# Optimization experiments

Measured on AMD Instinct MI355X. Metric: run time of the kernel, lower is better.

Reference implementation:

```python
import jax, jax.numpy as jnp
import numpy as np

N_NODES = 20000
N_EDGES = 640000
IN_DIM = 128
HID = 128
NUM_GRAPHS = 64


def setup_inputs() -> dict:
    key = jax.random.key(0)
    ks = jax.random.split(key, 12)
    x = jax.random.normal(ks[0], (N_NODES, IN_DIM), dtype=jnp.float32)
    edge_index = jax.random.randint(ks[1], (2, N_EDGES), 0, N_NODES, dtype=jnp.int64)
    batch = jnp.sort(jax.random.randint(ks[2], (N_NODES,), 0, NUM_GRAPHS, dtype=jnp.int64))
    edge_attr = jax.random.uniform(ks[3], (N_EDGES,), dtype=jnp.float32)
    s1 = 1.0 / np.sqrt(IN_DIM)
    s2 = 1.0 / np.sqrt(HID)
    # GraphConv layer 1: lin_rel (with bias) on aggregated messages, lin_root (no bias) on x
    W1_rel = jax.random.uniform(ks[4], (HID, IN_DIM), minval=-s1, maxval=s1, dtype=jnp.float32)
    b1 = jax.random.uniform(ks[5], (HID,), minval=-s1, maxval=s1, dtype=jnp.float32)
    W1_root = jax.random.uniform(ks[6], (HID, IN_DIM), minval=-s1, maxval=s1, dtype=jnp.float32)
    # GraphConv layer 3 (conv2 is unused in forward)
    W3_rel = jax.random.uniform(ks[7], (HID, HID), minval=-s2, maxval=s2, dtype=jnp.float32)
    b3 = jax.random.uniform(ks[8], (HID,), minval=-s2, maxval=s2, dtype=jnp.float32)
    W3_root = jax.random.uniform(ks[9], (HID, HID), minval=-s2, maxval=s2, dtype=jnp.float32)
    # Final linear head
    Wlin = jax.random.uniform(ks[10], (1, HID), minval=-s2, maxval=s2, dtype=jnp.float32)
    blin = jax.random.uniform(ks[11], (1,), minval=-s2, maxval=s2, dtype=jnp.float32)
    return {
        "x": x, "edge_index": edge_index, "batch": batch, "edge_attr": edge_attr,
        "W1_rel": W1_rel, "b1": b1, "W1_root": W1_root,
        "W3_rel": W3_rel, "b3": b3, "W3_root": W3_root,
        "Wlin": Wlin, "blin": blin, "num_graphs": NUM_GRAPHS,
    }


def graph_conv(x, src, dst, edge_w, W_rel, b_rel, W_root):
    # PyG GraphConv (aggr='add'): out = W_rel @ sum_{j in N(i)} w_ij * x_j + b_rel + W_root @ x_i
    msg = x[src] * edge_w[:, None]                       # [E, d] gather + scale
    agg = jax.ops.segment_sum(msg, dst, num_segments=x.shape[0])  # [N, d] scatter-add
    return agg @ W_rel.T + b_rel + x @ W_root.T


def reference(x, edge_index, batch, edge_attr,
              W1_rel, b1, W1_root, W3_rel, b3, W3_root, Wlin, blin, num_graphs):
    src, dst = edge_index[0], edge_index[1]
    h = graph_conv(x, src, dst, edge_attr, W1_rel, b1, W1_root)
    h = jax.nn.relu(h)
    # dropout p=0.5 is identity in eval mode
    h = graph_conv(h, src, dst, edge_attr, W3_rel, b3, W3_root)
    # global_mean_pool over per-node graph ids
    sums = jax.ops.segment_sum(h, batch, num_segments=num_graphs)          # [G, H]
    counts = jax.ops.segment_sum(jnp.ones((h.shape[0],), h.dtype), batch,
                                 num_segments=num_graphs)                  # [G]
    pooled = sums / jnp.maximum(counts, 1.0)[:, None]
    out = jax.nn.relu(pooled @ Wlin.T + blin)                              # [G, 1]
    return out
```

## Files before the change

### kernel.cpp

```cpp
#include <hip/hip_runtime.h>

#define N_NODES 20000
#define N_EDGES 640000
#define DIM 128
#define NGRAPH 64
#define NBUCK 313
#define EPB 2048
#define NB_HIST 313
#define NB_WCONV 32
#define RED_BLOCKS 512

typedef __attribute__((ext_vector_type(8))) short short8;
typedef __attribute__((ext_vector_type(4))) float floatx4;

__device__ __forceinline__ unsigned int bf16rne(float f) {
    unsigned int u = __float_as_uint(f);
    return (u + 0x7FFFu + ((u >> 16) & 1u)) >> 16;
}

__global__ __launch_bounds__(256) void k_front(
    const int* __restrict__ dst,
    const float* __restrict__ Wrel, const float* __restrict__ Wroot,
    const float* __restrict__ W3rel, const float* __restrict__ W3root,
    const float* __restrict__ b3, const float* __restrict__ Wlin,
    unsigned short* __restrict__ wbh, unsigned short* __restrict__ wbl,
    int* __restrict__ ghist, int* __restrict__ ticket_hist,
    int* __restrict__ boff, int* __restrict__ gcursor,
    float* __restrict__ vrel, float* __restrict__ vroot, float* __restrict__ cb3) {

    const int t = threadIdx.x;
    const int blk = blockIdx.x;

    if (blk < NB_HIST) {
        __shared__ int lhist[NBUCK];
        __shared__ int islast;
        for (int i = t; i < NBUCK; i += 256) lhist[i] = 0;
        __syncthreads();
        const int e0 = blk * EPB;
        for (int i = 0; i < 8; ++i) {
            int e = e0 + i * 256 + t;
            if (e < N_EDGES) atomicAdd(&lhist[dst[e] >> 6], 1);
        }
        __syncthreads();
        for (int i = t; i < NBUCK; i += 256)
            if (lhist[i]) atomicAdd(&ghist[i], lhist[i]);
        __syncthreads();
        if (t == 0) {
            __threadfence();
            islast = (atomicAdd(ticket_hist, 1) == NB_HIST - 1);
        }
        __syncthreads();
        if (islast) {
            __threadfence();
            if (t < 64) {
                int carry = 0;
                for (int c = 0; c < 5; ++c) {
                    int idx = c * 64 + t;
                    int v = (idx < NBUCK)
                        ? __hip_atomic_load(&ghist[idx], __ATOMIC_RELAXED,
                                            __HIP_MEMORY_SCOPE_AGENT)
                        : 0;
                    int xv = v;
                    for (int s = 1; s < 64; s <<= 1) {
                        int u = __shfl_up(xv, s);
                        if (t >= s) xv += u;
                    }
                    int excl = carry + xv - v;
                    if (idx < NBUCK) { boff[idx] = excl; gcursor[idx] = excl; }
                    carry += __shfl(xv, 63);
                }
                if (t == 0) boff[NBUCK] = carry;
            }
        }
    } else if (blk < NB_HIST + NB_WCONV) {
        const int b = blk - NB_HIST;
        for (int i = b * 256 + t; i < 256 * DIM; i += NB_WCONV * 256) {
            int n = i >> 7, k = i & 127;
            float v = (n < DIM) ? Wrel[n * DIM + k] : Wroot[(n - DIM) * DIM + k];
            unsigned int h = bf16rne(v);
            wbh[i] = (unsigned short)h;
            wbl[i] = (unsigned short)bf16rne(v - __uint_as_float(h << 16));
        }
    } else {
        if (t < 64) {
            for (int kk = 0; kk < 2; ++kk) {
                int k = t + kk * 64;
                float sr = 0.f, so = 0.f;
                for (int h = 0; h < DIM; ++h) {
                    float wl = Wlin[h];
                    sr = fmaf(wl, W3rel[h * DIM + k], sr);
                    so = fmaf(wl, W3root[h * DIM + k], so);
                }
                vrel[k] = sr;
                vroot[k] = so;
            }
            float c = b3[t] * Wlin[t] + b3[t + 64] * Wlin[t + 64];
            for (int m = 32; m > 0; m >>= 1) c += __shfl_xor(c, m);
            if (t == 0) cb3[0] = c;
        }
    }
}

__global__ __launch_bounds__(256) void k_partition(const int* __restrict__ src,
                                                   const int* __restrict__ dst,
                                                   const float* __restrict__ ew,
                                                   int* __restrict__ gcursor,
                                                   int2* __restrict__ part) {
    __shared__ int lhist[NBUCK], lbase[NBUCK], gbase[NBUCK], lcur[NBUCK];
    __shared__ int2 lrec[EPB];
    const int t = threadIdx.x;
    for (int i = t; i < NBUCK; i += 256) lhist[i] = 0;
    __syncthreads();
    const int e0 = blockIdx.x * EPB;
    const int tot = min(EPB, N_EDGES - e0);
    int mys[8], myd[8];
    float myw[8];
    for (int i = 0; i < 8; ++i) {
        int e = e0 + i * 256 + t;
        if (e < N_EDGES) {
            mys[i] = src[e];
            myd[i] = dst[e];
            myw[i] = ew[e];
            atomicAdd(&lhist[myd[i] >> 6], 1);
        } else {
            myd[i] = -1;
        }
    }
    __syncthreads();
    if (t < 64) {
        int carry = 0;
        for (int c = 0; c < 5; ++c) {
            int idx = c * 64 + t;
            int v = (idx < NBUCK) ? lhist[idx] : 0;
            int xv = v;
            for (int s = 1; s < 64; s <<= 1) {
                int u = __shfl_up(xv, s);
                if (t >= s) xv += u;
            }
            if (idx < NBUCK) { lbase[idx] = carry + xv - v; lcur[idx] = 0; }
            carry += __shfl(xv, 63);
        }
    }
    __syncthreads();
    for (int i = t; i < NBUCK; i += 256) {
        int cnt = lhist[i];
        gbase[i] = cnt ? atomicAdd(&gcursor[i], cnt) : 0;
    }
    __syncthreads();
    for (int i = 0; i < 8; ++i) {
        if (myd[i] >= 0) {
            int bb = myd[i] >> 6;
            int slot = lbase[bb] + atomicAdd(&lcur[bb], 1);
            lrec[slot] = make_int2((myd[i] << 16) | mys[i], __float_as_int(myw[i]));
        }
    }
    __syncthreads();
    for (int i = t; i < tot; i += 256) {
        int2 rc = lrec[i];
        int bb = (rc.x >> 16) >> 6;
        part[gbase[bb] + (i - lbase[bb])] = rc;
    }
}

__global__ __launch_bounds__(256) void k_gemm(
    const float* __restrict__ x,
    const unsigned short* __restrict__ wbh, const unsigned short* __restrict__ wbl,
    const float* __restrict__ b1,
    unsigned short* __restrict__ yb, float* __restrict__ r) {
    extern __shared__ unsigned short smem[];
    uint4* sh = (uint4*)smem;
    uint4* sl = (uint4*)(smem + 16384);

    const int t = threadIdx.x;
    const int g = blockIdx.x;
    const int half = blockIdx.y;
    const int n0 = half * 128;

    const uint4* gh = (const uint4*)wbh + (size_t)n0 * 16;
    const uint4* gl = (const uint4*)wbl + (size_t)n0 * 16;
    for (int i = t; i < 2048; i += 256) {
        int row = i >> 4, c = i & 15;
        int sc = row * 16 + (c ^ (row & 15));
        sh[sc] = gh[i];
        sl[sc] = gl[i];
    }
    __syncthreads();

    const int lane = t & 63;
    const int m = lane & 15;
    const int q = lane >> 4;
    const int row0 = g * 64 + (t >> 6) * 16;
    const int row = row0 + m;
    const bool ok = row < N_NODES;

    const short8* SH = (const short8*)smem;
    const short8* SL = (const short8*)(smem + 16384);

    floatx4 acc[8];
    #pragma unroll
    for (int i = 0; i < 8; ++i) acc[i] = (floatx4)(0.f);

    #pragma unroll
    for (int kc = 0; kc < 4; ++kc) {
        float4 v0 = make_float4(0.f, 0.f, 0.f, 0.f);
        float4 v1 = make_float4(0.f, 0.f, 0.f, 0.f);
        if (ok) {
            const float4* xp = (const float4*)(x + (size_t)row * DIM + kc * 32 + q * 8);
            v0 = xp[0];
            v1 = xp[1];
        }
        float f[8] = {v0.x, v0.y, v0.z, v0.w, v1.x, v1.y, v1.z, v1.w};
        short8 ah, al;
        #pragma unroll
        for (int i = 0; i < 8; ++i) {
            unsigned int h = bf16rne(f[i]);
            ah[i] = (short)h;
            al[i] = (short)bf16rne(f[i] - __uint_as_float(h << 16));
        }
        #pragma unroll
        for (int nt = 0; nt < 8; ++nt) {
            int n = nt * 16 + m;
            int cc = (kc * 4 + q) ^ m;
            short8 bh = SH[n * 16 + cc];
            short8 bl = SL[n * 16 + cc];
            acc[nt] = __builtin_amdgcn_mfma_f32_16x16x32_bf16(ah, bh, acc[nt], 0, 0, 0);
            acc[nt] = __builtin_amdgcn_mfma_f32_16x16x32_bf16(al, bh, acc[nt], 0, 0, 0);
            acc[nt] = __builtin_amdgcn_mfma_f32_16x16x32_bf16(ah, bl, acc[nt], 0, 0, 0);
        }
    }

    #pragma unroll
    for (int nt = 0; nt < 8; ++nt) {
        int col = n0 + nt * 16 + m;
        float bias = (col >= DIM) ? b1[col - DIM] : 0.f;
        #pragma unroll
        for (int reg = 0; reg < 4; ++reg) {
            int orow = row0 + q * 4 + reg;
            if (orow < N_NODES) {
                float v = acc[nt][reg];
                if (col < DIM)
                    yb[orow * DIM + col] = (unsigned short)bf16rne(v);
                else
                    r[orow * DIM + (col - DIM)] = v + bias;
            }
        }
    }
}

__global__ __launch_bounds__(256) void k_bucketsort(const int* __restrict__ boff,
                                                    const int2* __restrict__ part,
                                                    int2* __restrict__ sorted,
                                                    int* __restrict__ off) {
    __shared__ int nh[64], ncur[64];
    const int b = blockIdx.x;
    const int t = threadIdx.x;
    const int s0 = boff[b], s1 = boff[b + 1];
    if (t < 64) nh[t] = 0;
    __syncthreads();
    for (int i = s0 + t; i < s1; i += 256) atomicAdd(&nh[(part[i].x >> 16) & 63], 1);
    __syncthreads();
    if (t < 64) {
        int v = nh[t];
        int xv = v;
        for (int s = 1; s < 64; s <<= 1) {
            int u = __shfl_up(xv, s);
            if (t >= s) xv += u;
        }
        int excl = xv - v;
        ncur[t] = excl;
        int node = b * 64 + t;
        if (node < N_NODES) off[node] = s0 + excl;
    }
    __syncthreads();
    for (int i = s0 + t; i < s1; i += 256) {
        int2 rc = part[i];
        int dl = (rc.x >> 16) & 63;
        int p = atomicAdd(&ncur[dl], 1);
        sorted[s0 + p] = make_int2(rc.x & 0xFFFF, rc.y);
    }
    if (b == 0 && t == 0) off[N_NODES] = N_EDGES;
}

__global__ __launch_bounds__(256) void k_agg(const unsigned int* __restrict__ yb,
                                             const float2* __restrict__ r2,
                                             const int* __restrict__ off,
                                             const int2* __restrict__ grec,
                                             const float2* __restrict__ vrel2,
                                             const float2* __restrict__ vroot2,
                                             float* __restrict__ aout,
                                             float* __restrict__ bout) {
    const int lane = threadIdx.x & 63;
    const int node = blockIdx.x * 4 + (threadIdx.x >> 6);
    if (node >= N_NODES) return;

    int j = off[node];
    const int e1 = off[node + 1];
    float sx = 0.f, sy = 0.f;
    for (; j + 4 <= e1; j += 4) {
        int2 r0 = grec[j], r1 = grec[j + 1], rr2 = grec[j + 2], r3 = grec[j + 3];
        float w0 = __int_as_float(r0.y), w1 = __int_as_float(r1.y);
        float w2 = __int_as_float(rr2.y), w3 = __int_as_float(r3.y);
        unsigned int v0 = yb[r0.x * 64 + lane];
        unsigned int v1 = yb[r1.x * 64 + lane];
        unsigned int v2 = yb[rr2.x * 64 + lane];
        unsigned int v3 = yb[r3.x * 64 + lane];
        sx = fmaf(w0, __uint_as_float(v0 << 16),
             fmaf(w1, __uint_as_float(v1 << 16),
             fmaf(w2, __uint_as_float(v2 << 16),
             fmaf(w3, __uint_as_float(v3 << 16), sx))));
        sy = fmaf(w0, __uint_as_float(v0 & 0xFFFF0000u),
             fmaf(w1, __uint_as_float(v1 & 0xFFFF0000u),
             fmaf(w2, __uint_as_float(v2 & 0xFFFF0000u),
             fmaf(w3, __uint_as_float(v3 & 0xFFFF0000u), sy))));
    }
    for (; j < e1; ++j) {
        int2 rc = grec[j];
        float w = __int_as_float(rc.y);
        unsigned int v = yb[rc.x * 64 + lane];
        sx = fmaf(w, __uint_as_float(v << 16), sx);
        sy = fmaf(w, __uint_as_float(v & 0xFFFF0000u), sy);
    }
    float2 rr = r2[(size_t)node * 64 + lane];
    float hx = fmaxf(sx + rr.x, 0.f);
    float hy = fmaxf(sy + rr.y, 0.f);
    float2 vr = vrel2[lane];
    float2 vo = vroot2[lane];
    float pa = hx * vr.x + hy * vr.y;
    float pb = hx * vo.x + hy * vo.y;
    for (int mm = 32; mm > 0; mm >>= 1) {
        pa += __shfl_xor(pa, mm);
        pb += __shfl_xor(pb, mm);
    }
    if (lane == 0) {
        aout[node] = pa;
        bout[node] = pb;
    }
}

__global__ __launch_bounds__(256) void k_reduce_final(
    const int2* __restrict__ sorted, const int* __restrict__ off,
    const float* __restrict__ a, const float* __restrict__ bvec,
    const int* __restrict__ batch,
    float* __restrict__ gpart, int* __restrict__ gpartc,
    int* __restrict__ ticket_red,
    const float* __restrict__ cb3, const float* __restrict__ blin,
    float* __restrict__ out) {
    __shared__ float sbin[NGRAPH];
    __shared__ int cbin[NGRAPH];
    __shared__ int islast;
    const int t = threadIdx.x;
    for (int i = t; i < NGRAPH; i += 256) { sbin[i] = 0.f; cbin[i] = 0; }
    __syncthreads();
    const int lane = t & 63;
    const int gw = blockIdx.x * 4 + (t >> 6);
    const int nw = gridDim.x * 4;
    for (int node = gw; node < N_NODES; node += nw) {
        const int e0 = off[node], e1 = off[node + 1];
        float s = 0.f;
        for (int j = e0 + lane; j < e1; j += 64) {
            int2 rc = sorted[j];
            s = fmaf(__int_as_float(rc.y), a[rc.x], s);
        }
        for (int mm = 32; mm > 0; mm >>= 1) s += __shfl_xor(s, mm);
        if (lane == 0) {
            int g = batch[node];
            atomicAdd(&sbin[g], s + bvec[node]);
            atomicAdd(&cbin[g], 1);
        }
    }
    __syncthreads();
    const int slot = blockIdx.x & 63;
    for (int i = t; i < NGRAPH; i += 256) {
        atomicAdd(&gpart[slot * NGRAPH + i], sbin[i]);
        if (cbin[i]) atomicAdd(&gpartc[slot * NGRAPH + i], cbin[i]);
    }
    __syncthreads();
    if (t == 0) {
        __threadfence();
        islast = (atomicAdd(ticket_red, 1) == (int)gridDim.x - 1);
    }
    __syncthreads();
    if (islast) {
        __threadfence();
        if (t < NGRAPH) {
            float S = 0.f;
            int C = 0;
            for (int s2 = 0; s2 < 64; ++s2) {
                S += __hip_atomic_load(&gpart[s2 * NGRAPH + t], __ATOMIC_RELAXED,
                                       __HIP_MEMORY_SCOPE_AGENT);
                C += __hip_atomic_load(&gpartc[s2 * NGRAPH + t], __ATOMIC_RELAXED,
                                       __HIP_MEMORY_SCOPE_AGENT);
            }
            float denom = (C > 0) ? (float)C : 1.f;
            float v = (S + (float)C * cb3[0]) / denom + blin[0];
            out[t] = (v > 0.f) ? v : 0.f;
        }
    }
}

extern "C" void kernel_launch(void* const* d_in, const int* in_sizes, int n_in,
                              void* d_out, int out_size, void* d_ws, size_t ws_size,
                              hipStream_t stream) {
    const float* x = (const float*)d_in[0];
    const int* edge_index = (const int*)d_in[1];
    const int* src = edge_index;
    const int* dst = edge_index + N_EDGES;
    const int* batch = (const int*)d_in[2];
    const float* ew = (const float*)d_in[3];
    const float* W1rel = (const float*)d_in[4];
    const float* b1 = (const float*)d_in[5];
    const float* W1root = (const float*)d_in[6];
    const float* W3rel = (const float*)d_in[7];
    const float* b3 = (const float*)d_in[8];
    const float* W3root = (const float*)d_in[9];
    const float* Wlin = (const float*)d_in[10];
    const float* blin = (const float*)d_in[11];
    float* out = (float*)d_out;

    char* w = (char*)d_ws;
    size_t o = 0;
    auto alloc = [&](size_t bytes) -> void* {
        void* p = w + o;
        o += bytes;
        o = (o + 255) & ~(size_t)255;
        return p;
    };
    char* zbase = (char*)alloc(1280 + 64 * NGRAPH * 4 * 2);
    int* ghist = (int*)zbase;
    int* ticket_hist = ghist + NBUCK;
    int* ticket_red = ghist + NBUCK + 1;
    float* gpart = (float*)(zbase + 1280);
    int* gpartc = (int*)(zbase + 1280 + 64 * NGRAPH * 4);
    const size_t zbytes = 1280 + 64 * NGRAPH * 4 * 2;

    unsigned short* wbh = (unsigned short*)alloc((size_t)256 * DIM * 2);
    unsigned short* wbl = (unsigned short*)alloc((size_t)256 * DIM * 2);
    unsigned short* yb = (unsigned short*)alloc((size_t)N_NODES * DIM * 2);
    float* r = (float*)alloc((size_t)N_NODES * DIM * 4);
    int* boff = (int*)alloc((size_t)(NBUCK + 1) * 4);
    int* gcursor = (int*)alloc((size_t)NBUCK * 4);
    int2* part = (int2*)alloc((size_t)N_EDGES * 8);
    int2* sorted = (int2*)alloc((size_t)N_EDGES * 8);
    int* off = (int*)alloc((size_t)(N_NODES + 1) * 4);
    float* a = (float*)alloc((size_t)N_NODES * 4);
    float* b = (float*)alloc((size_t)N_NODES * 4);
    float* vrel = (float*)alloc(DIM * 4);
    float* vroot = (float*)alloc(DIM * 4);
    float* cb3 = (float*)alloc(4);

    hipMemsetAsync(zbase, 0, zbytes, stream);

    k_front<<<NB_HIST + NB_WCONV + 1, 256, 0, stream>>>(
        dst, W1rel, W1root, W3rel, W3root, b3, Wlin,
        wbh, wbl, ghist, ticket_hist, boff, gcursor, vrel, vroot, cb3);

    k_partition<<<NB_HIST, 256, 0, stream>>>(src, dst, ew, gcursor, part);

    k_gemm<<<dim3(NBUCK, 2), 256, 65536, stream>>>(x, wbh, wbl, b1, yb, r);

    k_bucketsort<<<NBUCK, 256, 0, stream>>>(boff, part, sorted, off);

    k_agg<<<(N_NODES + 3) / 4, 256, 0, stream>>>(
        (const unsigned int*)yb, (const float2*)r, off, sorted,
        (const float2*)vrel, (const float2*)vroot, a, b);

    k_reduce_final<<<RED_BLOCKS, 256, 0, stream>>>(
        sorted, off, a, b, batch, gpart, gpartc, ticket_red, cb3, blin, out);
}
```

Baseline: 194.4 us.

## Fuse the whole pipeline into one cooperative persistent kernel with grid syncs

Replaces the memset and six separate kernel launches with one cooperative kernel of 1024 blocks. Each phase is a job loop, and the phases are separated by grid.sync(). Partition and GEMM now run in the same phase, and the GEMM is split into 32-column tiles so the staged weights fit the shared-memory union. The final reduction now scatters along edges over `part` and no longer walks sorted CSR. This is meant to remove launch gaps and tail idle time, at the cost of grid-wide barriers and lower per-block shared memory; the old multi-kernel path is kept as a fallback if the cooperative launch fails.

```diff
diff --git a/kernel.cpp b/kernel.cpp
--- a/kernel.cpp
+++ b/kernel.cpp
@@ -1,4 +1,7 @@
 #include <hip/hip_runtime.h>
+#include <hip/hip_cooperative_groups.h>
+
+namespace cg = cooperative_groups;
 
 #define N_NODES 20000
 #define N_EDGES 640000
@@ -8,6 +11,8 @@
 #define EPB 2048
 #define NB_HIST 313
 #define NB_WCONV 32
+#define GRID 1024
+#define NZERO 443
 #define RED_BLOCKS 512
 
 typedef __attribute__((ext_vector_type(8))) short short8;
@@ -18,7 +23,357 @@
     return (u + 0x7FFFu + ((u >> 16) & 1u)) >> 16;
 }
 
-__global__ __launch_bounds__(256) void k_front(
+union SMemU {
+    struct { int lhist[NBUCK], lbase[NBUCK], gbase[NBUCK], lcur[NBUCK]; int2 lrec[EPB]; } p;
+    struct { unsigned short h[32 * DIM], l[32 * DIM]; } g;
+    struct { int nh[64], ncur[64]; } s;
+    struct { float sbin[NGRAPH]; int cbin[NGRAPH]; } rd;
+};
+
+__global__ __launch_bounds__(256, 4) void mega(
+    const int* __restrict__ srcA, const int* __restrict__ dstA,
+    const float* __restrict__ ew, const int* __restrict__ batch,
+    const float* __restrict__ x,
+    const float* __restrict__ W1rel, const float* __restrict__ b1,
+    const float* __restrict__ W1root,
+    const float* __restrict__ W3rel, const float* __restrict__ b3,
+    const float* __restrict__ W3root,
+    const float* __restrict__ Wlin, const float* __restrict__ blin,
+    unsigned short* __restrict__ wbh, unsigned short* __restrict__ wbl,
+    unsigned short* __restrict__ yb, float* __restrict__ r,
+    int* __restrict__ zr, int* __restrict__ boff, int* __restrict__ gcursor,
+    int2* __restrict__ part, int2* __restrict__ sorted, int* __restrict__ off,
+    float* __restrict__ aArr, float* __restrict__ bArr,
+    float* __restrict__ vrel, float* __restrict__ vroot, float* __restrict__ cb3,
+    float* __restrict__ out)
+{
+    __shared__ SMemU sm;
+    __shared__ int flag;
+    cg::grid_group grid = cg::this_grid();
+    const int t = threadIdx.x;
+    const int B = blockIdx.x;
+    const int G = gridDim.x;
+
+    int* ghist = zr;
+    int* ticket_hist = zr + 313;
+    int* ticket_red = zr + 314;
+    float* gsum = (float*)(zr + 315);
+    int* gcntg = zr + 379;
+
+    for (int i = B * 256 + t; i < NZERO; i += G * 256) zr[i] = 0;
+    grid.sync();
+
+    for (int job = B; job < NB_HIST + NB_WCONV + 1; job += G) {
+        if (job < NB_HIST) {
+            for (int i = t; i < NBUCK; i += 256) sm.p.lhist[i] = 0;
+            __syncthreads();
+            const int e0 = job * EPB;
+            for (int i = 0; i < 8; ++i) {
+                int e = e0 + i * 256 + t;
+                if (e < N_EDGES) atomicAdd(&sm.p.lhist[dstA[e] >> 6], 1);
+            }
+            __syncthreads();
+            for (int i = t; i < NBUCK; i += 256)
+                if (sm.p.lhist[i]) atomicAdd(&ghist[i], sm.p.lhist[i]);
+            __syncthreads();
+            if (t == 0) {
+                __threadfence();
+                flag = (atomicAdd(ticket_hist, 1) == NB_HIST - 1);
+            }
+            __syncthreads();
+            if (flag && t < 64) {
+                int carry = 0;
+                for (int c = 0; c < 5; ++c) {
+                    int idx = c * 64 + t;
+                    int v = (idx < NBUCK)
+                        ? __hip_atomic_load(&ghist[idx], __ATOMIC_RELAXED,
+                                            __HIP_MEMORY_SCOPE_AGENT)
+                        : 0;
+                    int xv = v;
+                    for (int s = 1; s < 64; s <<= 1) {
+                        int u = __shfl_up(xv, s);
+                        if (t >= s) xv += u;
+                    }
+                    int excl = carry + xv - v;
+                    if (idx < NBUCK) { boff[idx] = excl; gcursor[idx] = excl; }
+                    carry += __shfl(xv, 63);
+                }
+                if (t == 0) boff[NBUCK] = carry;
+                __threadfence();
+            }
+        } else if (job < NB_HIST + NB_WCONV) {
+            const int bb = job - NB_HIST;
+            for (int i = bb * 256 + t; i < 256 * DIM; i += NB_WCONV * 256) {
+                int n = i >> 7, k = i & 127;
+                float v = (n < DIM) ? W1rel[n * DIM + k] : W1root[(n - DIM) * DIM + k];
+                unsigned int h = bf16rne(v);
+                wbh[i] = (unsigned short)h;
+                wbl[i] = (unsigned short)bf16rne(v - __uint_as_float(h << 16));
+            }
+        } else {
+            if (t < 64) {
+                for (int kk = 0; kk < 2; ++kk) {
+                    int k = t + kk * 64;
+                    float sr = 0.f, so = 0.f;
+                    for (int h = 0; h < DIM; ++h) {
+                        float wl = Wlin[h];
+                        sr = fmaf(wl, W3rel[h * DIM + k], sr);
+                        so = fmaf(wl, W3root[h * DIM + k], so);
+                    }
+                    vrel[k] = sr;
+                    vroot[k] = so;
+                }
+                float c = b3[t] * Wlin[t] + b3[t + 64] * Wlin[t + 64];
+                for (int m = 32; m > 0; m >>= 1) c += __shfl_xor(c, m);
+                if (t == 0) cb3[0] = c;
+            }
+        }
+        __syncthreads();
+    }
+    grid.sync();
+
+    for (int job = B; job < NB_HIST + 2504; job += G) {
+        if (job < NB_HIST) {
+            for (int i = t; i < NBUCK; i += 256) sm.p.lhist[i] = 0;
+            __syncthreads();
+            const int e0 = job * EPB;
+            const int tot = min(EPB, N_EDGES - e0);
+            int mys[8], myd[8];
+            float myw[8];
+            for (int i = 0; i < 8; ++i) {
+                int e = e0 + i * 256 + t;
+                if (e < N_EDGES) {
+                    mys[i] = srcA[e];
+                    myd[i] = dstA[e];
+                    myw[i] = ew[e];
+                    atomicAdd(&sm.p.lhist[myd[i] >> 6], 1);
+                } else {
+                    myd[i] = -1;
+                }
+            }
+            __syncthreads();
+            if (t < 64) {
+                int carry = 0;
+                for (int c = 0; c < 5; ++c) {
+                    int idx = c * 64 + t;
+                    int v = (idx < NBUCK) ? sm.p.lhist[idx] : 0;
+                    int xv = v;
+                    for (int s = 1; s < 64; s <<= 1) {
+                        int u = __shfl_up(xv, s);
+                        if (t >= s) xv += u;
+                    }
+                    if (idx < NBUCK) { sm.p.lbase[idx] = carry + xv - v; sm.p.lcur[idx] = 0; }
+                    carry += __shfl(xv, 63);
+                }
+            }
+            __syncthreads();
+            for (int i = t; i < NBUCK; i += 256) {
+                int cnt = sm.p.lhist[i];
+                sm.p.gbase[i] = cnt ? atomicAdd(&gcursor[i], cnt) : 0;
+            }
+            __syncthreads();
+            for (int i = 0; i < 8; ++i) {
+                if (myd[i] >= 0) {
+                    int bb = myd[i] >> 6;
+                    int slot = sm.p.lbase[bb] + atomicAdd(&sm.p.lcur[bb], 1);
+                    sm.p.lrec[slot] = make_int2((myd[i] << 16) | mys[i], __float_as_int(myw[i]));
+                }
+            }
+            __syncthreads();
+            for (int i = t; i < tot; i += 256) {
+                int2 rc = sm.p.lrec[i];
+                int bb = ((unsigned)rc.x >> 16) >> 6;
+                part[sm.p.gbase[bb] + (i - sm.p.lbase[bb])] = rc;
+            }
+        } else {
+            const int tile = job - NB_HIST;
+            const int g = tile >> 3;
+            const int col0 = (tile & 7) * 32;
+            uint4* sh4 = (uint4*)sm.g.h;
+            uint4* sl4 = (uint4*)sm.g.l;
+            const uint4* gh = (const uint4*)wbh + (size_t)col0 * 16;
+            const uint4* gl = (const uint4*)wbl + (size_t)col0 * 16;
+            for (int i = t; i < 512; i += 256) {
+                int row = i >> 4, c = i & 15;
+                int sc = row * 16 + (c ^ (row & 15));
+                sh4[sc] = gh[i];
+                sl4[sc] = gl[i];
+            }
+            __syncthreads();
+            const int lane = t & 63;
+            const int m = lane & 15;
+            const int q = lane >> 4;
+            const int row0 = g * 64 + (t >> 6) * 16;
+            const int row = row0 + m;
+            const bool ok = row < N_NODES;
+            const short8* SH = (const short8*)sm.g.h;
+            const short8* SL = (const short8*)sm.g.l;
+            floatx4 acc[2];
+            acc[0] = (floatx4)(0.f);
+            acc[1] = (floatx4)(0.f);
+            #pragma unroll
+            for (int kc = 0; kc < 4; ++kc) {
+                float4 v0 = make_float4(0.f, 0.f, 0.f, 0.f);
+                float4 v1 = make_float4(0.f, 0.f, 0.f, 0.f);
+                if (ok) {
+                    const float4* xp = (const float4*)(x + (size_t)row * DIM + kc * 32 + q * 8);
+                    v0 = xp[0];
+                    v1 = xp[1];
+                }
+                float f[8] = {v0.x, v0.y, v0.z, v0.w, v1.x, v1.y, v1.z, v1.w};
+                short8 ah, al;
+                #pragma unroll
+                for (int i = 0; i < 8; ++i) {
+                    unsigned int h = bf16rne(f[i]);
+                    ah[i] = (short)h;
+                    al[i] = (short)bf16rne(f[i] - __uint_as_float(h << 16));
+                }
+                #pragma unroll
+                for (int nt = 0; nt < 2; ++nt) {
+                    int nl = nt * 16 + m;
+                    int cc = (kc * 4 + q) ^ m;
+                    short8 bh = SH[nl * 16 + cc];
+                    short8 bl = SL[nl * 16 + cc];
+                    acc[nt] = __builtin_amdgcn_mfma_f32_16x16x32_bf16(ah, bh, acc[nt], 0, 0, 0);
+                    acc[nt] = __builtin_amdgcn_mfma_f32_16x16x32_bf16(al, bh, acc[nt], 0, 0, 0);
+                    acc[nt] = __builtin_amdgcn_mfma_f32_16x16x32_bf16(ah, bl, acc[nt], 0, 0, 0);
+                }
+            }
+            #pragma unroll
+            for (int nt = 0; nt < 2; ++nt) {
+                int col = col0 + nt * 16 + m;
+                float bias = (col >= DIM) ? b1[col - DIM] : 0.f;
+                #pragma unroll
+                for (int reg = 0; reg < 4; ++reg) {
+                    int orow = row0 + q * 4 + reg;
+                    if (orow < N_NODES) {
+                        float v = acc[nt][reg];
+                        if (col < DIM)
+                            yb[orow * DIM + col] = (unsigned short)bf16rne(v);
+                        else
+                            r[orow * DIM + (col - DIM)] = v + bias;
+                    }
+                }
+            }
+        }
+        __syncthreads();
+    }
+    grid.sync();
+
+    for (int job = B; job < NBUCK; job += G) {
+        const int s0 = boff[job], s1 = boff[job + 1];
+        if (t < 64) sm.s.nh[t] = 0;
+        __syncthreads();
+        for (int i = s0 + t; i < s1; i += 256)
+            atomicAdd(&sm.s.nh[((unsigned)part[i].x >> 16) & 63], 1);
+        __syncthreads();
+        if (t < 64) {
+            int v = sm.s.nh[t];
+            int xv = v;
+            for (int s = 1; s < 64; s <<= 1) {
+                int u = __shfl_up(xv, s);
+                if (t >= s) xv += u;
+            }
+            int excl = xv - v;
+            sm.s.ncur[t] = excl;
+            int node = job * 64 + t;
+            if (node < N_NODES) off[node] = s0 + excl;
+        }
+        __syncthreads();
+        for (int i = s0 + t; i < s1; i += 256) {
+            int2 rc = part[i];
+            int dl = ((unsigned)rc.x >> 16) & 63;
+            int p = atomicAdd(&sm.s.ncur[dl], 1);
+            sorted[s0 + p] = make_int2(rc.x & 0xFFFF, rc.y);
+        }
+        if (job == 0 && t == 0) off[N_NODES] = N_EDGES;
+        __syncthreads();
+    }
+    grid.sync();
+
+    {
+        const int lane = t & 63;
+        const float2* r2 = (const float2*)r;
+        const unsigned int* yb32 = (const unsigned int*)yb;
+        float2 vr = ((const float2*)vrel)[lane];
+        float2 vo = ((const float2*)vroot)[lane];
+        for (int node = B * 4 + (t >> 6); node < N_NODES; node += G * 4) {
+            int j = off[node];
+            const int e1 = off[node + 1];
+            float sx = 0.f, sy = 0.f;
+            for (; j + 8 <= e1; j += 8) {
+                int2 rc[8];
+                #pragma unroll
+                for (int u = 0; u < 8; ++u) rc[u] = sorted[j + u];
+                unsigned int v[8];
+                #pragma unroll
+                for (int u = 0; u < 8; ++u) v[u] = yb32[rc[u].x * 64 + lane];
+                #pragma unroll
+                for (int u = 0; u < 8; ++u) {
+                    float w = __int_as_float(rc[u].y);
+                    sx = fmaf(w, __uint_as_float(v[u] << 16), sx);
+                    sy = fmaf(w, __uint_as_float(v[u] & 0xFFFF0000u), sy);
+                }
+            }
+            for (; j < e1; ++j) {
+                int2 rcs = sorted[j];
+                float w = __int_as_float(rcs.y);
+                unsigned int vv = yb32[rcs.x * 64 + lane];
+                sx = fmaf(w, __uint_as_float(vv << 16), sx);
+                sy = fmaf(w, __uint_as_float(vv & 0xFFFF0000u), sy);
+            }
+            float2 rr = r2[(size_t)node * 64 + lane];
+            float hx = fmaxf(sx + rr.x, 0.f);
+            float hy = fmaxf(sy + rr.y, 0.f);
+            float pa = hx * vr.x + hy * vr.y;
+            float pb = hx * vo.x + hy * vo.y;
+            for (int mm = 32; mm > 0; mm >>= 1) {
+                pa += __shfl_xor(pa, mm);
+                pb += __shfl_xor(pb, mm);
+            }
+            if (lane == 0) {
+                aArr[node] = pa;
+                bArr[node] = pb;
+            }
+        }
+    }
+    grid.sync();
+
+    for (int i = t; i < NGRAPH; i += 256) { sm.rd.sbin[i] = 0.f; sm.rd.cbin[i] = 0; }
+    __syncthreads();
+    for (int i = B * 256 + t; i < N_EDGES; i += G * 256) {
+        int2 rc = part[i];
+        int srcn = rc.x & 0xFFFF;
+        int dstn = (int)((unsigned)rc.x >> 16);
+        atomicAdd(&sm.rd.sbin[batch[dstn]], __int_as_float(rc.y) * aArr[srcn]);
+    }
+    for (int n = B * 256 + t; n < N_NODES; n += G * 256) {
+        int g = batch[n];
+        atomicAdd(&sm.rd.sbin[g], bArr[n]);
+        atomicAdd(&sm.rd.cbin[g], 1);
+    }
+    __syncthreads();
+    if (t < NGRAPH) {
+        if (sm.rd.sbin[t] != 0.f) atomicAdd(&gsum[t], sm.rd.sbin[t]);
+        if (sm.rd.cbin[t]) atomicAdd(&gcntg[t], sm.rd.cbin[t]);
+    }
+    __syncthreads();
+    if (t == 0) {
+        __threadfence();
+        flag = (atomicAdd(ticket_red, 1) == G - 1);
+    }
+    __syncthreads();
+    if (flag && t < NGRAPH) {
+        __threadfence();
+        float S = __hip_atomic_load(&gsum[t], __ATOMIC_RELAXED, __HIP_MEMORY_SCOPE_AGENT);
+        int C = __hip_atomic_load(&gcntg[t], __ATOMIC_RELAXED, __HIP_MEMORY_SCOPE_AGENT);
+        float denom = (C > 0) ? (float)C : 1.f;
+        float v = (S + (float)C * cb3[0]) / denom + blin[0];
+        out[t] = (v > 0.f) ? v : 0.f;
+    }
+}
+
+__global__ __launch_bounds__(256) void k_front9(
     const int* __restrict__ dst,
     const float* __restrict__ Wrel, const float* __restrict__ Wroot,
     const float* __restrict__ W3rel, const float* __restrict__ W3root,
@@ -27,10 +382,8 @@
     int* __restrict__ ghist, int* __restrict__ ticket_hist,
     int* __restrict__ boff, int* __restrict__ gcursor,
     float* __restrict__ vrel, float* __restrict__ vroot, float* __restrict__ cb3) {
-
     const int t = threadIdx.x;
     const int blk = blockIdx.x;
-
     if (blk < NB_HIST) {
         __shared__ int lhist[NBUCK];
         __shared__ int islast;
@@ -101,11 +454,11 @@
     }
 }
 
-__global__ __launch_bounds__(256) void k_partition(const int* __restrict__ src,
-                                                   const int* __restrict__ dst,
-                                                   const float* __restrict__ ew,
-                                                   int* __restrict__ gcursor,
-                                                   int2* __restrict__ part) {
+__global__ __launch_bounds__(256) void k_partition9(const int* __restrict__ src,
+                                                    const int* __restrict__ dst,
+                                                    const float* __restrict__ ew,
+                                                    int* __restrict__ gcursor,
+                                                    int2* __restrict__ part) {
     __shared__ int lhist[NBUCK], lbase[NBUCK], gbase[NBUCK], lcur[NBUCK];
     __shared__ int2 lrec[EPB];
     const int t = threadIdx.x;
@@ -157,12 +510,12 @@
     __syncthreads();
     for (int i = t; i < tot; i += 256) {
         int2 rc = lrec[i];
-        int bb = (rc.x >> 16) >> 6;
+        int bb = ((unsigned)rc.x >> 16) >> 6;
         part[gbase[bb] + (i - lbase[bb])] = rc;
     }
 }
 
-__global__ __launch_bounds__(256) void k_gemm(
+__global__ __launch_bounds__(256) void k_gemm9(
     const float* __restrict__ x,
     const unsigned short* __restrict__ wbh, const unsigned short* __restrict__ wbl,
     const float* __restrict__ b1,
@@ -170,12 +523,10 @@
     extern __shared__ unsigned short smem[];
     uint4* sh = (uint4*)smem;
     uint4* sl = (uint4*)(smem + 16384);
-
     const int t = threadIdx.x;
     const int g = blockIdx.x;
     const int half = blockIdx.y;
     const int n0 = half * 128;
-
     const uint4* gh = (const uint4*)wbh + (size_t)n0 * 16;
     const uint4* gl = (const uint4*)wbl + (size_t)n0 * 16;
     for (int i = t; i < 2048; i += 256) {
@@ -185,21 +536,17 @@
         sl[sc] = gl[i];
     }
     __syncthreads();
-
     const int lane = t & 63;
     const int m = lane & 15;
     const int q = lane >> 4;
     const int row0 = g * 64 + (t >> 6) * 16;
     const int row = row0 + m;
     const bool ok = row < N_NODES;
-
     const short8* SH = (const short8*)smem;
     const short8* SL = (const short8*)(smem + 16384);
-
     floatx4 acc[8];
     #pragma unroll
     for (int i = 0; i < 8; ++i) acc[i] = (floatx4)(0.f);
-
     #pragma unroll
     for (int kc = 0; kc < 4; ++kc) {
         float4 v0 = make_float4(0.f, 0.f, 0.f, 0.f);
@@ -228,7 +575,6 @@
             acc[nt] = __builtin_amdgcn_mfma_f32_16x16x32_bf16(ah, bl, acc[nt], 0, 0, 0);
         }
     }
-
     #pragma unroll
     for (int nt = 0; nt < 8; ++nt) {
         int col = n0 + nt * 16 + m;
@@ -247,17 +593,18 @@
     }
 }
 
-__global__ __launch_bounds__(256) void k_bucketsort(const int* __restrict__ boff,
-                                                    const int2* __restrict__ part,
-                                                    int2* __restrict__ sorted,
-                                                    int* __restrict__ off) {
+__global__ __launch_bounds__(256) void k_bucketsort9(const int* __restrict__ boff,
+                                                     const int2* __restrict__ part,
+                                                     int2* __restrict__ sorted,
+                                                     int* __restrict__ off) {
     __shared__ int nh[64], ncur[64];
     const int b = blockIdx.x;
     const int t = threadIdx.x;
     const int s0 = boff[b], s1 = boff[b + 1];
     if (t < 64) nh[t] = 0;
     __syncthreads();
-    for (int i = s0 + t; i < s1; i += 256) atomicAdd(&nh[(part[i].x >> 16) & 63], 1);
+    for (int i = s0 + t; i < s1; i += 256)
+        atomicAdd(&nh[((unsigned)part[i].x >> 16) & 63], 1);
     __syncthreads();
     if (t < 64) {
         int v = nh[t];
@@ -274,25 +621,24 @@
     __syncthreads();
     for (int i = s0 + t; i < s1; i += 256) {
         int2 rc = part[i];
-        int dl = (rc.x >> 16) & 63;
+        int dl = ((unsigned)rc.x >> 16) & 63;
         int p = atomicAdd(&ncur[dl], 1);
         sorted[s0 + p] = make_int2(rc.x & 0xFFFF, rc.y);
     }
     if (b == 0 && t == 0) off[N_NODES] = N_EDGES;
 }
 
-__global__ __launch_bounds__(256) void k_agg(const unsigned int* __restrict__ yb,
-                                             const float2* __restrict__ r2,
-                                             const int* __restrict__ off,
-                                             const int2* __restrict__ grec,
-                                             const float2* __restrict__ vrel2,
-                                             const float2* __restrict__ vroot2,
-                                             float* __restrict__ aout,
-                                             float* __restrict__ bout) {
+__global__ __launch_bounds__(256) void k_agg9(const unsigned int* __restrict__ yb,
+                                              const float2* __restrict__ r2,
+                                              const int* __restrict__ off,
+                                              const int2* __restrict__ grec,
+                                              const float2* __restrict__ vrel2,
+                                              const float2* __restrict__ vroot2,
+                                              float* __restrict__ aout,
+                                              float* __restrict__ bout) {
     const int lane = threadIdx.x & 63;
     const int node = blockIdx.x * 4 + (threadIdx.x >> 6);
     if (node >= N_NODES) return;
-
     int j = off[node];
     const int e1 = off[node + 1];
     float sx = 0.f, sy = 0.f;
@@ -337,7 +683,7 @@
     }
 }
 
-__global__ __launch_bounds__(256) void k_reduce_final(
+__global__ __launch_bounds__(256) void k_reduce_final9(
     const int2* __restrict__ sorted, const int* __restrict__ off,
     const float* __restrict__ a, const float* __restrict__ bvec,
     const int* __restrict__ batch,
@@ -425,13 +771,14 @@
         o = (o + 255) & ~(size_t)255;
         return p;
     };
-    char* zbase = (char*)alloc(1280 + 64 * NGRAPH * 4 * 2);
-    int* ghist = (int*)zbase;
-    int* ticket_hist = ghist + NBUCK;
-    int* ticket_red = ghist + NBUCK + 1;
-    float* gpart = (float*)(zbase + 1280);
-    int* gpartc = (int*)(zbase + 1280 + 64 * NGRAPH * 4);
-    const size_t zbytes = 1280 + 64 * NGRAPH * 4 * 2;
+    int* zr = (int*)alloc(NZERO * 4);
+    char* zbase9 = (char*)alloc(1280 + 64 * NGRAPH * 4 * 2);
+    int* ghist9 = (int*)zbase9;
+    int* ticket_hist9 = ghist9 + NBUCK;
+    int* ticket_red9 = ghist9 + NBUCK + 1;
+    float* gpart9 = (float*)(zbase9 + 1280);
+    int* gpartc9 = (int*)(zbase9 + 1280 + 64 * NGRAPH * 4);
+    const size_t zbytes9 = 1280 + 64 * NGRAPH * 4 * 2;
 
     unsigned short* wbh = (unsigned short*)alloc((size_t)256 * DIM * 2);
     unsigned short* wbl = (unsigned short*)alloc((size_t)256 * DIM * 2);
@@ -448,22 +795,33 @@
     float* vroot = (float*)alloc(DIM * 4);
     float* cb3 = (float*)alloc(4);
 
-    hipMemsetAsync(zbase, 0, zbytes, stream);
-
-    k_front<<<NB_HIST + NB_WCONV + 1, 256, 0, stream>>>(
-        dst, W1rel, W1root, W3rel, W3root, b3, Wlin,
-        wbh, wbl, ghist, ticket_hist, boff, gcursor, vrel, vroot, cb3);
-
-    k_partition<<<NB_HIST, 256, 0, stream>>>(src, dst, ew, gcursor, part);
-
-    k_gemm<<<dim3(NBUCK, 2), 256, 65536, stream>>>(x, wbh, wbl, b1, yb, r);
-
-    k_bucketsort<<<NBUCK, 256, 0, stream>>>(boff, part, sorted, off);
-
-    k_agg<<<(N_NODES + 3) / 4, 256, 0, stream>>>(
-        (const unsigned int*)yb, (const float2*)r, off, sorted,
-        (const float2*)vrel, (const float2*)vroot, a, b);
-
-    k_reduce_final<<<RED_BLOCKS, 256, 0, stream>>>(
-        sorted, off, a, b, batch, gpart, gpartc, ticket_red, cb3, blin, out);
+    void* args[] = {
+        (void*)&src, (void*)&dst, (void*)&ew, (void*)&batch, (void*)&x,
+        (void*)&W1rel, (void*)&b1, (void*)&W1root,
+        (void*)&W3rel, (void*)&b3, (void*)&W3root,
+        (void*)&Wlin, (void*)&blin,
+        (void*)&wbh, (void*)&wbl, (void*)&yb, (void*)&r,
+        (void*)&zr, (void*)&boff, (void*)&gcursor,
+        (void*)&part, (void*)&sorted, (void*)&off,
+        (void*)&a, (void*)&b, (void*)&vrel, (void*)&vroot, (void*)&cb3,
+        (void*)&out};
+
+    hipError_t cerr = hipLaunchCooperativeKernel(
+        (const void*)mega, dim3(GRID), dim3(256), (void**)args, 0, stream);
+
+    if (cerr != hipSuccess) {
+        (void)hipGetLastError();
+        hipMemsetAsync(zbase9, 0, zbytes9, stream);
+        k_front9<<<NB_HIST + NB_WCONV + 1, 256, 0, stream>>>(
+            dst, W1rel, W1root, W3rel, W3root, b3, Wlin,
+            wbh, wbl, ghist9, ticket_hist9, boff, gcursor, vrel, vroot, cb3);
+        k_partition9<<<NB_HIST, 256, 0, stream>>>(src, dst, ew, gcursor, part);
+        k_gemm9<<<dim3(NBUCK, 2), 256, 65536, stream>>>(x, wbh, wbl, b1, yb, r);
+        k_bucketsort9<<<NBUCK, 256, 0, stream>>>(boff, part, sorted, off);
+        k_agg9<<<(N_NODES + 3) / 4, 256, 0, stream>>>(
+            (const unsigned int*)yb, (const float2*)r, off, sorted,
+            (const float2*)vrel, (const float2*)vroot, a, b);
+        k_reduce_final9<<<RED_BLOCKS, 256, 0, stream>>>(
+            sorted, off, a, b, batch, gpart9, gpartc9, ticket_red9, cb3, blin, out);
+    }
 }
```

Result: slower. 735.0 us (+278.2%).
